# Performance work log

Hardware: AMD Instinct MI355X
Metric: run time of the kernel (lower is better)

The kernel has to match this reference:

```python
import jax, jax.numpy as jnp
import numpy as np

N_ATOMS = 8_388_608
N_MOL = 65_536
FIDELITY_LEVEL = 1
FIDELITY_OFFSET = 200
SAE_SIZE = 518  # (fidelity_level+1)*offset + 118


def setup_inputs() -> dict:
    key = jax.random.key(0)
    k1, k2, k3, k4 = jax.random.split(key, 4)
    numbers = jax.random.randint(k1, (N_ATOMS,), 0, 119, dtype=jnp.int32)
    mol_idx = jnp.sort(jax.random.randint(k2, (N_ATOMS,), 0, N_MOL, dtype=jnp.int32))
    energy = jax.random.normal(k3, (N_MOL,), dtype=jnp.float32)
    sae_tensor = jax.random.normal(k4, (SAE_SIZE,), dtype=jnp.float32)
    return {"energy": energy, "sae_tensor": sae_tensor, "numbers": numbers, "mol_idx": mol_idx}


def reference(energy, sae_tensor, numbers, mol_idx):
    # embedding-style gather: per-atom SAE energy at shifted atomic number
    shifted = numbers + FIDELITY_LEVEL * FIDELITY_OFFSET
    sae_per_atom = sae_tensor[shifted]  # [N_ATOMS]
    # per-molecule segment sum (replaces the Python loop over molecules)
    sae_energy = jax.ops.segment_sum(sae_per_atom, mol_idx, num_segments=N_MOL)  # [N_MOL]
    return energy + sae_energy
```

## Files before the change

### kernel.cpp

```cpp
#include <hip/hip_runtime.h>


#define SAE_WINDOW 119
#define SAE_SHIFT  200

__global__ __launch_bounds__(256)
void sae_segsum_kernel(const float* __restrict__ sae,
                       const int*   __restrict__ numbers,
                       const int*   __restrict__ mol_idx,
                       float*       __restrict__ out,
                       int n_vec4, int stride)
{
    __shared__ float s_sae[128];
    const int tid  = threadIdx.x;
    if (tid < SAE_WINDOW) s_sae[tid] = sae[SAE_SHIFT + tid];
    __syncthreads();

    const int lane = tid & 63;
    const int gtid = blockIdx.x * blockDim.x + tid;

    const int4* __restrict__ num4 = (const int4*)numbers;
    const int4* __restrict__ mol4 = (const int4*)mol_idx;

    const int iters = (n_vec4 + stride - 1) / stride;

    for (int it = 0; it < iters; ++it) {
        const int i = gtid + it * stride;
        int   key = -1;
        float val = 0.0f;

        if (i < n_vec4) {
            const int4 n = num4[i];
            const int4 m = mol4[i];
            const float v0 = s_sae[n.x];
            const float v1 = s_sae[n.y];
            const float v2 = s_sae[n.z];
            const float v3 = s_sae[n.w];

            int cur = m.x; float acc = v0;
            if (m.y == cur) acc += v1; else { atomicAdd(&out[cur], acc); cur = m.y; acc = v1; }
            if (m.z == cur) acc += v2; else { atomicAdd(&out[cur], acc); cur = m.z; acc = v2; }
            if (m.w == cur) acc += v3; else { atomicAdd(&out[cur], acc); cur = m.w; acc = v3; }
            key = cur; val = acc;
        }

        #pragma unroll
        for (int d = 1; d < 64; d <<= 1) {
            const int   okey = __shfl_down(key, d, 64);
            const float oval = __shfl_down(val, d, 64);
            if ((lane + d) < 64 && okey == key) val += oval;
        }
        const int pkey = __shfl_up(key, 1, 64);
        if (key >= 0 && (lane == 0 || pkey != key)) {
            atomicAdd(&out[key], val);
        }
    }
}

__global__ void sae_tail_kernel(const float* __restrict__ sae,
                                const int*   __restrict__ numbers,
                                const int*   __restrict__ mol_idx,
                                float*       __restrict__ out,
                                int start, int n_atoms)
{
    int i = start + blockIdx.x * blockDim.x + threadIdx.x;
    if (i < n_atoms) {
        atomicAdd(&out[mol_idx[i]], sae[numbers[i] + SAE_SHIFT]);
    }
}

extern "C" void kernel_launch(void* const* d_in, const int* in_sizes, int n_in,
                              void* d_out, int out_size, void* d_ws, size_t ws_size,
                              hipStream_t stream) {
    const float* energy  = (const float*)d_in[0];
    const float* sae     = (const float*)d_in[1];
    const int*   numbers = (const int*)d_in[2];
    const int*   mol_idx = (const int*)d_in[3];
    float*       out     = (float*)d_out;

    const int n_atoms = in_sizes[2];
    const int n_vec4  = n_atoms >> 2;

    hipMemcpyAsync(out, energy, (size_t)out_size * sizeof(float),
                   hipMemcpyDeviceToDevice, stream);

    const int block  = 256;
    const int grid   = 2048;
    const int stride = grid * block;

    sae_segsum_kernel<<<grid, block, 0, stream>>>(sae, numbers, mol_idx, out,
                                                  n_vec4, stride);

    const int rem = n_atoms & 3;
    if (rem) {
        sae_tail_kernel<<<1, 64, 0, stream>>>(sae, numbers, mol_idx, out,
                                              n_vec4 << 2, n_atoms);
    }
}
```

Measured before the change: 100.5 us.

## Process 16 atoms per thread and replicate SAE table across LDS banks

```diff
diff --git a/kernel.cpp b/kernel.cpp
--- a/kernel.cpp
+++ b/kernel.cpp
@@ -9,39 +9,72 @@
                        const int*   __restrict__ numbers,
                        const int*   __restrict__ mol_idx,
                        float*       __restrict__ out,
-                       int n_vec4, int stride)
+                       int n_vec4, int n_chunks, int stride)
 {
-    __shared__ float s_sae[128];
-    const int tid  = threadIdx.x;
-    if (tid < SAE_WINDOW) s_sae[tid] = sae[SAE_SHIFT + tid];
+    __shared__ float s_sae[SAE_WINDOW * 32];
+    const int tid = threadIdx.x;
+    for (int idx = tid; idx < SAE_WINDOW * 32; idx += 256)
+        s_sae[idx] = sae[SAE_SHIFT + (idx >> 5)];
     __syncthreads();
 
     const int lane = tid & 63;
-    const int gtid = blockIdx.x * blockDim.x + tid;
+    const float* __restrict__ s_lane = s_sae + (lane & 31);
 
     const int4* __restrict__ num4 = (const int4*)numbers;
     const int4* __restrict__ mol4 = (const int4*)mol_idx;
 
-    const int iters = (n_vec4 + stride - 1) / stride;
+    const int gtid  = blockIdx.x * blockDim.x + tid;
+    const int iters = (n_chunks + stride - 1) / stride;
 
     for (int it = 0; it < iters; ++it) {
-        const int i = gtid + it * stride;
+        const int c = gtid + it * stride;
+
         int   key = -1;
         float val = 0.0f;
 
-        if (i < n_vec4) {
-            const int4 n = num4[i];
-            const int4 m = mol4[i];
-            const float v0 = s_sae[n.x];
-            const float v1 = s_sae[n.y];
-            const float v2 = s_sae[n.z];
-            const float v3 = s_sae[n.w];
+        if (c < n_chunks) {
+            const int base = c << 2;
 
-            int cur = m.x; float acc = v0;
-            if (m.y == cur) acc += v1; else { atomicAdd(&out[cur], acc); cur = m.y; acc = v1; }
-            if (m.z == cur) acc += v2; else { atomicAdd(&out[cur], acc); cur = m.z; acc = v2; }
-            if (m.w == cur) acc += v3; else { atomicAdd(&out[cur], acc); cur = m.w; acc = v3; }
-            key = cur; val = acc;
+            int4 nv[4], mv[4];
+            #pragma unroll
+            for (int j = 0; j < 4; ++j) {
+                if (base + j < n_vec4) {
+                    nv[j] = num4[base + j];
+                    mv[j] = mol4[base + j];
+                } else {
+                    nv[j] = make_int4(0, 0, 0, 0);
+                    mv[j] = make_int4(-1, -1, -1, -1);
+                }
+            }
+
+            int   cur = mv[0].x;
+            float acc = s_lane[nv[0].x << 5];
+
+            #define MERGE_STEP(mk, nk)                                    \
+                do {                                                      \
+                    const int   _m = (mk);                                \
+                    const float _v = s_lane[(nk) << 5];                   \
+                    if (_m == cur) acc += _v;                             \
+                    else {                                                \
+                        if (cur >= 0) atomicAdd(&out[cur], acc);          \
+                        cur = _m; acc = _v;                               \
+                    }                                                     \
+                } while (0)
+
+            MERGE_STEP(mv[0].y, nv[0].y);
+            MERGE_STEP(mv[0].z, nv[0].z);
+            MERGE_STEP(mv[0].w, nv[0].w);
+            #pragma unroll
+            for (int j = 1; j < 4; ++j) {
+                MERGE_STEP(mv[j].x, nv[j].x);
+                MERGE_STEP(mv[j].y, nv[j].y);
+                MERGE_STEP(mv[j].z, nv[j].z);
+                MERGE_STEP(mv[j].w, nv[j].w);
+            }
+            #undef MERGE_STEP
+
+            key = cur;
+            val = acc;
         }
 
         #pragma unroll
@@ -78,18 +111,20 @@
     const int*   mol_idx = (const int*)d_in[3];
     float*       out     = (float*)d_out;
 
-    const int n_atoms = in_sizes[2];
-    const int n_vec4  = n_atoms >> 2;
+    const int n_atoms  = in_sizes[2];
+    const int n_vec4   = n_atoms >> 2;
+    const int n_chunks = (n_vec4 + 3) >> 2;
 
     hipMemcpyAsync(out, energy, (size_t)out_size * sizeof(float),
                    hipMemcpyDeviceToDevice, stream);
 
-    const int block  = 256;
-    const int grid   = 2048;
+    const int block = 256;
+    int grid = (n_chunks + block - 1) / block;
+    if (grid > 2048) grid = 2048;
     const int stride = grid * block;
 
     sae_segsum_kernel<<<grid, block, 0, stream>>>(sae, numbers, mol_idx, out,
-                                                  n_vec4, stride);
+                                                  n_vec4, n_chunks, stride);
 
     const int rem = n_atoms & 3;
     if (rem) {
```

Measured after the change: 107.3 us. 1.07x slower.
